# Kernel tuning notes

Hardware: AMD Instinct MI355X
Metric: run time of the kernel (lower is better)

## Reference

```python
import jax, jax.numpy as jnp
import numpy as np

B, S, D = 64, 2048, 512

def setup_inputs() -> dict:
    key = jax.random.key(0)
    k1, k2, k3, k4, k5 = jax.random.split(key, 5)
    x = jax.random.normal(k1, (B, S, D), dtype=jnp.float32)
    # torch Linear(dim, dim): weight [D, D], bias [D]
    W1 = jax.random.normal(k2, (D, D), dtype=jnp.float32) * (1.0 / np.sqrt(D))
    b1 = jax.random.normal(k3, (D,), dtype=jnp.float32) * 0.01
    # torch Linear(dim, 1): weight [1, D] -> stored as [D], bias scalar
    w2 = jax.random.normal(k4, (D,), dtype=jnp.float32) * (1.0 / np.sqrt(D))
    b2 = jax.random.normal(k5, (), dtype=jnp.float32) * 0.01
    return {"x": x, "W1": W1, "b1": b1, "w2": w2, "b2": b2}

def reference(x, W1, b1, w2, b2):
    # score MLP: Linear -> Tanh -> Linear(->1), squeeze
    h = jnp.tanh(jnp.einsum('bsd,ed->bse', x, W1) + b1)   # [B,S,D]
    scores = jnp.einsum('bsd,d->bs', h, w2) + b2          # [B,S]
    w = jax.nn.softmax(scores, axis=1)[..., None]         # [B,S,1]
    ctx = jnp.sum(x * w, axis=1)                          # [B,D]
    return (ctx, w)
```

## Files before the change

kernel.cpp:

```cpp
#include <hip/hip_runtime.h>
#include <hip/hip_bf16.h>

#define BB 64
#define SS 2048
#define DD 512
#define MTOT (BB * SS)

typedef __attribute__((ext_vector_type(8))) short short8;
typedef __attribute__((ext_vector_type(8))) unsigned short ushort8;
typedef __attribute__((ext_vector_type(4))) float f32x4;

__device__ __forceinline__ unsigned short f2bf(float f){
  union { float f; unsigned int u; } a; a.f = f;
  unsigned int r = a.u + 0x7fffu + ((a.u >> 16) & 1u);
  return (unsigned short)(r >> 16);
}

__device__ __forceinline__ ushort8 pack8(float4 a, float4 b){
  ushort8 u;
  u[0]=f2bf(a.x); u[1]=f2bf(a.y); u[2]=f2bf(a.z); u[3]=f2bf(a.w);
  u[4]=f2bf(b.x); u[5]=f2bf(b.y); u[6]=f2bf(b.z); u[7]=f2bf(b.w);
  return u;
}

__device__ __forceinline__ void gload_lds16(const unsigned short* g, unsigned short* l){
  __builtin_amdgcn_global_load_lds(
      (const __attribute__((address_space(1))) unsigned int*)g,
      (__attribute__((address_space(3))) unsigned int*)l, 16, 0, 0);
}

__global__ void cvt_w1_kernel(const float* __restrict__ W1, unsigned short* __restrict__ W1s){
  int i = blockIdx.x * blockDim.x + threadIdx.x;
  int s  = i >> 11;
  int g  = i & 2047;
  int kc = g >> 9;
  int e  = (g & 511) ^ kc;
  const float* src = W1 + (size_t)e * DD + s * 32 + kc * 8;
  float4 f0 = *(const float4*)src;
  float4 f1 = *(const float4*)(src + 4);
  *(ushort8*)(W1s + (size_t)i * 8) = pack8(f0, f1);
}

__launch_bounds__(512, 4)
__global__ void scores_kernel(const float* __restrict__ x,
                              const unsigned short* __restrict__ W1s,
                              const float* __restrict__ b1,
                              const float* __restrict__ w2,
                              float* __restrict__ scorep){
  __shared__ __align__(16) unsigned short lds[2][18432];

  const int t    = threadIdx.x;
  const int lane = t & 63;
  const int wid  = t >> 6;
  const int m0   = blockIdx.x * 64;
  const int arow = lane & 15;
  const int kgrp = lane >> 4;

  f32x4 acc[4][4];
  #pragma unroll
  for (int mt = 0; mt < 4; ++mt)
    #pragma unroll
    for (int et = 0; et < 4; ++et)
      acc[mt][et] = (f32x4){0.f, 0.f, 0.f, 0.f};

  const int srow = t >> 2;
  const int skc  = t & 3;
  const float* asrc0 = x + (size_t)(m0 + srow) * DD + skc * 8;
  const int awoff = ((skc << 6) + (srow ^ skc)) << 4;

  const unsigned short* bsrc0 = W1s + ((size_t)((wid << 2) << 6) + lane) * 8;

  #pragma unroll
  for (int j = 0; j < 4; ++j)
    gload_lds16(bsrc0 + j * 512, &lds[0][2048 + ((wid << 2) + j) * 512]);
  if (t < 256){
    float4 f0 = *(const float4*)asrc0;
    float4 f1 = *(const float4*)(asrc0 + 4);
    *(ushort8*)((char*)&lds[0][0] + awoff) = pack8(f0, f1);
  }
  __syncthreads();

  for (int s = 0; s < 16; ++s){
    unsigned short* cur = &lds[s & 1][0];
    unsigned short* nxt = &lds[(s + 1) & 1][0];

    float4 f0, f1;
    if (s < 15){
      const unsigned short* bs = bsrc0 + (size_t)(s + 1) * 16384;
      #pragma unroll
      for (int j = 0; j < 4; ++j)
        gload_lds16(bs + j * 512, nxt + 2048 + ((wid << 2) + j) * 512);
      if (t < 256){
        const float* as = asrc0 + (s + 1) * 32;
        f0 = *(const float4*)as;
        f1 = *(const float4*)(as + 4);
      }
    }

    short8 af[4], bf[4];
    #pragma unroll
    for (int mt = 0; mt < 4; ++mt){
      int row = mt * 16 + arow;
      af[mt] = *(const short8*)((char*)cur + (((kgrp << 6) + (row ^ kgrp)) << 4));
    }
    #pragma unroll
    for (int et = 0; et < 4; ++et){
      int e = (wid << 6) + (et << 4) + arow;
      bf[et] = *(const short8*)((char*)cur + 4096 + (((kgrp << 9) + (e ^ kgrp)) << 4));
    }

    __builtin_amdgcn_s_setprio(1);
    #pragma unroll
    for (int mt = 0; mt < 4; ++mt)
      #pragma unroll
      for (int et = 0; et < 4; ++et)
        acc[mt][et] = __builtin_amdgcn_mfma_f32_16x16x32_bf16(af[mt], bf[et], acc[mt][et], 0, 0, 0);
    __builtin_amdgcn_s_setprio(0);

    if (s < 15 && t < 256)
      *(ushort8*)((char*)nxt + awoff) = pack8(f0, f1);

    __syncthreads();
  }

  float ps[4][4];
  #pragma unroll
  for (int mt = 0; mt < 4; ++mt)
    #pragma unroll
    for (int i = 0; i < 4; ++i) ps[mt][i] = 0.f;

  #pragma unroll
  for (int et = 0; et < 4; ++et){
    int e = (wid << 6) + (et << 4) + arow;
    float b1v = b1[e];
    float w2v = w2[e];
    #pragma unroll
    for (int mt = 0; mt < 4; ++mt){
      #pragma unroll
      for (int i = 0; i < 4; ++i){
        float g = acc[mt][et][i] + b1v;
        g = fminf(15.f, fmaxf(-15.f, g));
        float ex = __expf(2.f * g);
        ps[mt][i] += (1.f - 2.f / (ex + 1.f)) * w2v;
      }
    }
  }
  #pragma unroll
  for (int mt = 0; mt < 4; ++mt)
    #pragma unroll
    for (int i = 0; i < 4; ++i){
      float v = ps[mt][i];
      v += __shfl_xor(v, 1);
      v += __shfl_xor(v, 2);
      v += __shfl_xor(v, 4);
      v += __shfl_xor(v, 8);
      ps[mt][i] = v;
    }
  float* psum = (float*)&lds[0][0];
  if ((lane & 15) == 0){
    #pragma unroll
    for (int mt = 0; mt < 4; ++mt)
      #pragma unroll
      for (int i = 0; i < 4; ++i)
        psum[wid * 64 + mt * 16 + (lane >> 4) * 4 + i] = ps[mt][i];
  }
  __syncthreads();
  if (t < 64){
    float ssum = 0.f;
    #pragma unroll
    for (int w = 0; w < 8; ++w) ssum += psum[w * 64 + t];
    scorep[m0 + t] = ssum;
  }
}

__global__ void softmax_kernel(const float* __restrict__ scorep, float* __restrict__ wout){
  const int b = blockIdx.x;
  const int t = threadIdx.x;
  float v[8];
  #pragma unroll
  for (int i = 0; i < 8; ++i) v[i] = scorep[(size_t)b * SS + t + i * 256];
  float m = v[0];
  #pragma unroll
  for (int i = 1; i < 8; ++i) m = fmaxf(m, v[i]);
  #pragma unroll
  for (int msk = 32; msk >= 1; msk >>= 1) m = fmaxf(m, __shfl_xor(m, msk));
  __shared__ float redm[4], reds[4];
  if ((t & 63) == 0) redm[t >> 6] = m;
  __syncthreads();
  m = fmaxf(fmaxf(redm[0], redm[1]), fmaxf(redm[2], redm[3]));
  float s = 0.f;
  #pragma unroll
  for (int i = 0; i < 8; ++i){ v[i] = __expf(v[i] - m); s += v[i]; }
  #pragma unroll
  for (int msk = 32; msk >= 1; msk >>= 1) s += __shfl_xor(s, msk);
  if ((t & 63) == 0) reds[t >> 6] = s;
  __syncthreads();
  s = reds[0] + reds[1] + reds[2] + reds[3];
  float inv = 1.f / s;
  #pragma unroll
  for (int i = 0; i < 8; ++i) wout[(size_t)b * SS + t + i * 256] = v[i] * inv;
}

__global__ void ctx_partial_kernel(const float* __restrict__ x, const float* __restrict__ wout,
                                   float* __restrict__ ctxp){
  __shared__ float red[4][512];
  const int t   = threadIdx.x;
  const int sub = t >> 7;
  const int dt  = t & 127;
  const int b   = blockIdx.x >> 3;
  const int sc  = blockIdx.x & 7;
  const float* xb = x + (size_t)b * SS * DD;
  const int s0 = sc * 256 + sub * 64;
  float4 acc = {0.f, 0.f, 0.f, 0.f};
  for (int s = s0; s < s0 + 64; ++s){
    float wv = wout[(size_t)b * SS + s];
    float4 xv = *(const float4*)(xb + (size_t)s * DD + dt * 4);
    acc.x += wv * xv.x; acc.y += wv * xv.y; acc.z += wv * xv.z; acc.w += wv * xv.w;
  }
  *(float4*)&red[sub][dt * 4] = acc;
  __syncthreads();
  if (t < 128){
    float4 r0 = *(const float4*)&red[0][t * 4];
    float4 r1 = *(const float4*)&red[1][t * 4];
    float4 r2 = *(const float4*)&red[2][t * 4];
    float4 r3 = *(const float4*)&red[3][t * 4];
    float4 o = { r0.x+r1.x+r2.x+r3.x, r0.y+r1.y+r2.y+r3.y,
                 r0.z+r1.z+r2.z+r3.z, r0.w+r1.w+r2.w+r3.w };
    *(float4*)&ctxp[((size_t)(b * 8 + sc)) * DD + t * 4] = o;
  }
}

__global__ void ctx_reduce_kernel(const float* __restrict__ ctxp, float* __restrict__ ctx){
  int i = blockIdx.x * blockDim.x + threadIdx.x;
  int b = i >> 9;
  int d = i & 511;
  float s = 0.f;
  #pragma unroll
  for (int sc = 0; sc < 8; ++sc) s += ctxp[((size_t)(b * 8 + sc)) * DD + d];
  ctx[(size_t)b * DD + d] = s;
}

extern "C" void kernel_launch(void* const* d_in, const int* in_sizes, int n_in,
                              void* d_out, int out_size, void* d_ws, size_t ws_size,
                              hipStream_t stream){
  const float* x  = (const float*)d_in[0];
  const float* W1 = (const float*)d_in[1];
  const float* b1 = (const float*)d_in[2];
  const float* w2 = (const float*)d_in[3];

  float* ctx  = (float*)d_out;
  float* wout = (float*)d_out + BB * DD;

  unsigned short* W1s = (unsigned short*)d_ws;
  float* scorep = (float*)((char*)d_ws + (512u << 10));
  float* ctxp   = (float*)d_ws;

  hipLaunchKernelGGL(cvt_w1_kernel,      dim3(128),  dim3(256), 0, stream, W1, W1s);
  hipLaunchKernelGGL(scores_kernel,      dim3(2048), dim3(512), 0, stream, x, W1s, b1, w2, scorep);
  hipLaunchKernelGGL(softmax_kernel,     dim3(64),   dim3(256), 0, stream, scorep, wout);
  hipLaunchKernelGGL(ctx_partial_kernel, dim3(512),  dim3(512), 0, stream, x, wout, ctxp);
  hipLaunchKernelGGL(ctx_reduce_kernel,  dim3(128),  dim3(256), 0, stream, ctxp, ctx);
}
```

Measured before the change: 163.0 us.

## Prefetch A two stages ahead with all threads and manual waitcnt barriers

Restructures the A-tile staging in the scores GEMM. All 512 threads now load 4 floats each instead of 256 threads loading 8, prefetching two k-steps ahead into registers, and the LDS layout gains a new row-major XOR swizzle. The __syncthreads is replaced with explicit vmcnt/lgkmcnt waits plus s_barrier, which lets one global load stay in flight across the barrier. The loop is fully unrolled and bf16 conversion now uses the HIP intrinsic. This aims to hide x load latency and spread the conversion work, at the cost of more registers and fragile hand-written waitcnt counting.

```diff
diff --git a/kernel.cpp b/kernel.cpp
--- a/kernel.cpp
+++ b/kernel.cpp
@@ -7,22 +7,24 @@
 #define MTOT (BB * SS)
 
 typedef __attribute__((ext_vector_type(8))) short short8;
-typedef __attribute__((ext_vector_type(8))) unsigned short ushort8;
+typedef __attribute__((ext_vector_type(4))) short s16x4;
 typedef __attribute__((ext_vector_type(4))) float f32x4;
 
-__device__ __forceinline__ unsigned short f2bf(float f){
-  union { float f; unsigned int u; } a; a.f = f;
-  unsigned int r = a.u + 0x7fffu + ((a.u >> 16) & 1u);
-  return (unsigned short)(r >> 16);
-}
-
-__device__ __forceinline__ ushort8 pack8(float4 a, float4 b){
-  ushort8 u;
+__device__ __forceinline__ short f2bf(float f){
+  __hip_bfloat16 h = __float2bfloat16(f);
+  return *reinterpret_cast<short*>(&h);
+}
+__device__ __forceinline__ short8 pack8(float4 a, float4 b){
+  short8 u;
   u[0]=f2bf(a.x); u[1]=f2bf(a.y); u[2]=f2bf(a.z); u[3]=f2bf(a.w);
   u[4]=f2bf(b.x); u[5]=f2bf(b.y); u[6]=f2bf(b.z); u[7]=f2bf(b.w);
   return u;
 }
-
+__device__ __forceinline__ s16x4 pack4(float4 a){
+  s16x4 u;
+  u[0]=f2bf(a.x); u[1]=f2bf(a.y); u[2]=f2bf(a.z); u[3]=f2bf(a.w);
+  return u;
+}
 __device__ __forceinline__ void gload_lds16(const unsigned short* g, unsigned short* l){
   __builtin_amdgcn_global_load_lds(
       (const __attribute__((address_space(1))) unsigned int*)g,
@@ -38,7 +40,7 @@
   const float* src = W1 + (size_t)e * DD + s * 32 + kc * 8;
   float4 f0 = *(const float4*)src;
   float4 f1 = *(const float4*)(src + 4);
-  *(ushort8*)(W1s + (size_t)i * 8) = pack8(f0, f1);
+  *(short8*)(W1s + (size_t)i * 8) = pack8(f0, f1);
 }
 
 __launch_bounds__(512, 4)
@@ -47,7 +49,9 @@
                               const float* __restrict__ b1,
                               const float* __restrict__ w2,
                               float* __restrict__ scorep){
-  __shared__ __align__(16) unsigned short lds[2][18432];
+  __shared__ __align__(16) unsigned short Bbuf[2][16384];
+  __shared__ __align__(16) unsigned short Abuf[2][2048];
+  __shared__ float psum[8 * 64];
 
   const int t    = threadIdx.x;
   const int lane = t & 63;
@@ -63,50 +67,48 @@
     for (int et = 0; et < 4; ++et)
       acc[mt][et] = (f32x4){0.f, 0.f, 0.f, 0.f};
 
-  const int srow = t >> 2;
-  const int skc  = t & 3;
-  const float* asrc0 = x + (size_t)(m0 + srow) * DD + skc * 8;
-  const int awoff = ((skc << 6) + (srow ^ skc)) << 4;
-
-  const unsigned short* bsrc0 = W1s + ((size_t)((wid << 2) << 6) + lane) * 8;
+  const int ar = t >> 3;
+  const int aq = t & 7;
+  const float* asrc = x + (size_t)(m0 + ar) * DD + aq * 4;
+  const int awoff = ((((ar << 2) + ((aq >> 1) ^ ((ar >> 1) & 3))) << 4) + ((aq & 1) << 3));
+
+  const unsigned short* bsrc = W1s + ((size_t)((wid << 2) << 6) + lane) * 8;
+
+  float4 areg[2];
 
   #pragma unroll
   for (int j = 0; j < 4; ++j)
-    gload_lds16(bsrc0 + j * 512, &lds[0][2048 + ((wid << 2) + j) * 512]);
-  if (t < 256){
-    float4 f0 = *(const float4*)asrc0;
-    float4 f1 = *(const float4*)(asrc0 + 4);
-    *(ushort8*)((char*)&lds[0][0] + awoff) = pack8(f0, f1);
-  }
-  __syncthreads();
-
+    gload_lds16(bsrc + j * 512, &Bbuf[0][((wid << 2) + j) * 512]);
+  float4 p0 = *(const float4*)asrc;
+  areg[1] = *(const float4*)(asrc + 32);
+  *(s16x4*)((char*)&Abuf[0][0] + awoff) = pack4(p0);
+  asm volatile("s_waitcnt vmcnt(1)" ::: "memory");
+  asm volatile("s_waitcnt lgkmcnt(0)" ::: "memory");
+  __builtin_amdgcn_s_barrier();
+  __builtin_amdgcn_sched_barrier(0);
+
+  #pragma unroll
   for (int s = 0; s < 16; ++s){
-    unsigned short* cur = &lds[s & 1][0];
-    unsigned short* nxt = &lds[(s + 1) & 1][0];
-
-    float4 f0, f1;
     if (s < 15){
-      const unsigned short* bs = bsrc0 + (size_t)(s + 1) * 16384;
+      const unsigned short* bs = bsrc + (size_t)(s + 1) * 16384;
       #pragma unroll
       for (int j = 0; j < 4; ++j)
-        gload_lds16(bs + j * 512, nxt + 2048 + ((wid << 2) + j) * 512);
-      if (t < 256){
-        const float* as = asrc0 + (s + 1) * 32;
-        f0 = *(const float4*)as;
-        f1 = *(const float4*)(as + 4);
-      }
-    }
+        gload_lds16(bs + j * 512, &Bbuf[(s + 1) & 1][((wid << 2) + j) * 512]);
+    }
+    if (s < 14)
+      areg[s & 1] = *(const float4*)(asrc + (s + 2) * 32);
 
     short8 af[4], bf[4];
     #pragma unroll
     for (int mt = 0; mt < 4; ++mt){
       int row = mt * 16 + arow;
-      af[mt] = *(const short8*)((char*)cur + (((kgrp << 6) + (row ^ kgrp)) << 4));
+      af[mt] = *(const short8*)((char*)&Abuf[s & 1][0]
+                + (((row << 2) + (kgrp ^ ((row >> 1) & 3))) << 4));
     }
     #pragma unroll
     for (int et = 0; et < 4; ++et){
       int e = (wid << 6) + (et << 4) + arow;
-      bf[et] = *(const short8*)((char*)cur + 4096 + (((kgrp << 9) + (e ^ kgrp)) << 4));
+      bf[et] = *(const short8*)((char*)&Bbuf[s & 1][0] + (((kgrp << 9) + (e ^ kgrp)) << 4));
     }
 
     __builtin_amdgcn_s_setprio(1);
@@ -117,10 +119,16 @@
         acc[mt][et] = __builtin_amdgcn_mfma_f32_16x16x32_bf16(af[mt], bf[et], acc[mt][et], 0, 0, 0);
     __builtin_amdgcn_s_setprio(0);
 
-    if (s < 15 && t < 256)
-      *(ushort8*)((char*)nxt + awoff) = pack8(f0, f1);
-
-    __syncthreads();
+    if (s < 15)
+      *(s16x4*)((char*)&Abuf[(s + 1) & 1][0] + awoff) = pack4(areg[(s + 1) & 1]);
+
+    if (s < 15){
+      if (s < 14) asm volatile("s_waitcnt vmcnt(1)" ::: "memory");
+      else        asm volatile("s_waitcnt vmcnt(0)" ::: "memory");
+      asm volatile("s_waitcnt lgkmcnt(0)" ::: "memory");
+      __builtin_amdgcn_s_barrier();
+      __builtin_amdgcn_sched_barrier(0);
+    }
   }
 
   float ps[4][4];
@@ -156,7 +164,6 @@
       v += __shfl_xor(v, 8);
       ps[mt][i] = v;
     }
-  float* psum = (float*)&lds[0][0];
   if ((lane & 15) == 0){
     #pragma unroll
     for (int mt = 0; mt < 4; ++mt)
```

New measurement: 169.2 us. +3.8%, slower.
